# Kernel tuning notes

Measured on AMD Instinct MI355X. Metric: run time of the kernel, lower is better.

Reference implementation:

```python
import jax, jax.numpy as jnp
import numpy as np

B, T, F, H, FW = 4096, 200, 32, 8, 5  # batch, seq, features, hidden, forward_size


def setup_inputs() -> dict:
    key = jax.random.key(0)
    ks = jax.random.split(key, 12)
    s_ih = 1.0 / np.sqrt(F + 1)
    s_hh = 1.0 / np.sqrt(H)
    inp = {
        "x": jax.random.normal(ks[0], (B, T, F), dtype=jnp.float32),
        "z0": jax.random.uniform(ks[1], (1, B, 1), dtype=jnp.float32),
        # LSTM cell over concat([x_t, z_{t-1}]) -> hidden 8, torch gate order i,f,g,o
        "W_ih": jax.random.uniform(ks[2], (4 * H, F + 1), minval=-s_ih, maxval=s_ih),
        "W_hh": jax.random.uniform(ks[3], (4 * H, H), minval=-s_hh, maxval=s_hh),
        "b_ih": jax.random.uniform(ks[4], (4 * H,), minval=-s_hh, maxval=s_hh),
        "b_hh": jax.random.uniform(ks[5], (4 * H,), minval=-s_hh, maxval=s_hh),
        # forward head: 8 -> 5 (relu, dropout inert at inference) -> 1 (relu, monotone increment)
        "W1": jax.random.uniform(ks[6], (FW, H), minval=-s_hh, maxval=s_hh),
        "b1": jax.random.uniform(ks[7], (FW,), minval=-s_hh, maxval=s_hh),
        "W2": jax.random.uniform(ks[8], (1, FW), minval=-1 / np.sqrt(FW), maxval=1 / np.sqrt(FW)),
        "b2": jax.random.uniform(ks[9], (1,), minval=-1 / np.sqrt(FW), maxval=1 / np.sqrt(FW)),
    }
    return inp


def _monotonic_lstm(x, z0, W_ih, W_hh, b_ih, b_hh, W1, b1, W2, b2):
    Bloc = x.shape[0]
    h0 = jnp.zeros((Bloc, H), x.dtype)
    c0 = jnp.zeros((Bloc, H), x.dtype)
    z = z0[0]  # (B, 1) : drop num_layers dim
    bias = b_ih + b_hh

    def step(carry, xt):
        h, c, z = carry
        inp = jnp.concatenate([xt, z], axis=-1)  # (B, F+1)
        gates = inp @ W_ih.T + h @ W_hh.T + bias  # (B, 4H)
        i, f, g, o = jnp.split(gates, 4, axis=-1)
        c = jax.nn.sigmoid(f) * c + jax.nn.sigmoid(i) * jnp.tanh(g)
        h = jax.nn.sigmoid(o) * jnp.tanh(c)
        d = jax.nn.relu(h @ W1.T + b1)            # dropout is identity at inference
        delta = jax.nn.relu(d @ W2.T + b2)        # nonnegative increment -> monotone z
        z = z + delta
        return (h, c, z), z

    _, zs = jax.lax.scan(step, (h0, c0, z), jnp.swapaxes(x, 0, 1))  # zs: (T, B, 1)
    return jnp.swapaxes(zs, 0, 1)  # (B, T, 1)


def reference(x, z0, W_ih, W_hh, b_ih, b_hh, W1, b1, W2, b2):
    return _monotonic_lstm(x, z0, W_ih, W_hh, b_ih, b_hh, W1, b1, W2, b2)
```

## Files before the change

kernel.cpp:

```cpp
#include <hip/hip_runtime.h>

#define T_LEN 200
#define F_IN  32
#define TC    8
#define NCH   (T_LEN / TC)
#define NB    4
#define PSTR  264
#define ZSTR  204

#define QP(a,b,c,d) ((a)|((b)<<2)|((c)<<4)|((d)<<6))
#define DPP_HM 0x141

typedef short  bf16x8  __attribute__((ext_vector_type(8)));
typedef float  floatx4 __attribute__((ext_vector_type(4)));

template <int CTRL>
__device__ __forceinline__ float dppf(float v) {
    return __int_as_float(__builtin_amdgcn_update_dpp(
        0, __float_as_int(v), CTRL, 0xF, 0xF, true));
}
__device__ __forceinline__ void bfsplit(float x, short& hi, short& lo) {
    unsigned u = __float_as_uint(x);
    unsigned short h = (unsigned short)(u >> 16);
    float fh = __uint_as_float(((unsigned)h) << 16);
    float r  = x - fh;
    hi = (short)h;
    lo = (short)(__float_as_uint(r) >> 16);
}

__launch_bounds__(128, 2)
__global__ void mono_lstm_kernel(const float* __restrict__ x,
                                 const float* __restrict__ z0,
                                 const float* __restrict__ W_ih,
                                 const float* __restrict__ W_hh,
                                 const float* __restrict__ b_ih,
                                 const float* __restrict__ b_hh,
                                 const float* __restrict__ W1,
                                 const float* __restrict__ b1,
                                 const float* __restrict__ W2,
                                 const float* __restrict__ b2,
                                 float* __restrict__ out) {
    __shared__ float pls[2 * NB * PSTR];
    __shared__ float zls[NB * ZSTR];

    const int tid  = threadIdx.x;
    const int lane = tid & 63;
    const int wv   = tid >> 6;
    const int bl   = (lane >> 3) & (NB - 1);
    const int j    = lane & 7;
    const int bg   = blockIdx.x * NB;

    const float L2E = 1.4426950408889634f;
    const float NSC = -L2E;
    const float NSG = -2.0f * L2E;

    const int n  = lane & 15;
    const int kq = lane >> 4;
    bf16x8 Bh0, Bl0, Bh1, Bl1;
    float bias0 = 0.f, bias1 = 0.f;

    const int   am  = lane & 15;
    const float* xa = x + ((size_t)(bg + (am >> 2)) * T_LEN + (am & 3)) * F_IN + kq * 8;

    float4 rgv[4];
    auto load_x = [&](int ch) {
#pragma unroll
        for (int s = 0; s < 2; ++s) {
            const float* p = xa + (size_t)(ch * TC + 4 * s) * F_IN;
            rgv[2 * s]     = *(const float4*)p;
            rgv[2 * s + 1] = *(const float4*)(p + 4);
        }
    };
    auto mfma_phase = [&](int buf) {
#pragma unroll
        for (int s = 0; s < 2; ++s) {
            const float xv[8] = {rgv[2*s].x, rgv[2*s].y, rgv[2*s].z, rgv[2*s].w,
                                 rgv[2*s+1].x, rgv[2*s+1].y, rgv[2*s+1].z, rgv[2*s+1].w};
            bf16x8 Ah, Al;
#pragma unroll
            for (int i = 0; i < 8; ++i) {
                short h, l;
                bfsplit(xv[i], h, l);
                Ah[i] = h; Al[i] = l;
            }
            floatx4 a0 = {bias0, bias0, bias0, bias0};
            floatx4 a1 = {bias1, bias1, bias1, bias1};
            a0 = __builtin_amdgcn_mfma_f32_16x16x32_bf16(Ah, Bh0, a0, 0, 0, 0);
            a0 = __builtin_amdgcn_mfma_f32_16x16x32_bf16(Al, Bh0, a0, 0, 0, 0);
            a0 = __builtin_amdgcn_mfma_f32_16x16x32_bf16(Ah, Bl0, a0, 0, 0, 0);
            a1 = __builtin_amdgcn_mfma_f32_16x16x32_bf16(Ah, Bh1, a1, 0, 0, 0);
            a1 = __builtin_amdgcn_mfma_f32_16x16x32_bf16(Al, Bh1, a1, 0, 0, 0);
            a1 = __builtin_amdgcn_mfma_f32_16x16x32_bf16(Ah, Bl1, a1, 0, 0, 0);
#pragma unroll
            for (int reg = 0; reg < 4; ++reg) {
                const int mr = (lane >> 4) * 4 + reg;
                const int bb = mr >> 2, tt = s * 4 + (mr & 3);
                pls[buf * NB * PSTR + bb * PSTR + tt * 32 + n]      = a0[reg];
                pls[buf * NB * PSTR + bb * PSTR + tt * 32 + 16 + n] = a1[reg];
            }
        }
    };

    float whi[8], whf[8], whg[8], who[8];
    float wzi = 0.f, wzf = 0.f, wzg = 0.f, wzo = 0.f;
    float w1h[5][8], b1v[5], w2v[5];
    float b2v = 0.f;
    float ha0 = 0.f, ha1 = 0.f, ha2 = 0.f, ha3 = 0.f,
          ha4 = 0.f, ha5 = 0.f, ha6 = 0.f, ha7 = 0.f;
    float c = 0.0f;
    float z = 0.f;

    if (wv == 1) {
        const int row0 = n, row1 = 16 + n;
        const float sc0 = NSC;
        const float sc1 = (n < 8) ? NSG : NSC;
#pragma unroll
        for (int i = 0; i < 8; ++i) {
            const int k = kq * 8 + i;
            short h, l;
            bfsplit(W_ih[row0 * 33 + k] * sc0, h, l); Bh0[i] = h; Bl0[i] = l;
            bfsplit(W_ih[row1 * 33 + k] * sc1, h, l); Bh1[i] = h; Bl1[i] = l;
        }
        bias0 = (b_ih[row0] + b_hh[row0]) * sc0;
        bias1 = (b_ih[row1] + b_hh[row1]) * sc1;

        load_x(0);
        mfma_phase(0);
        load_x(1);
    } else {
        const int ri = j, rf = 8 + j, rg_ = 16 + j, ro = 24 + j;
#pragma unroll
        for (int k = 0; k < 8; ++k) {
            whi[k] = W_hh[ri * 8 + (j ^ k)] * NSC;
            whf[k] = W_hh[rf * 8 + (j ^ k)] * NSC;
            whg[k] = W_hh[rg_ * 8 + (j ^ k)] * NSG;
            who[k] = W_hh[ro * 8 + (j ^ k)] * NSC;
        }
        wzi = W_ih[ri * 33 + 32] * NSC;
        wzf = W_ih[rf * 33 + 32] * NSC;
        wzg = W_ih[rg_ * 33 + 32] * NSG;
        wzo = W_ih[ro * 33 + 32] * NSC;

#pragma unroll
        for (int m = 0; m < 5; ++m) {
#pragma unroll
            for (int k = 0; k < 8; ++k) w1h[m][k] = W1[m * 8 + (j ^ k)];
            b1v[m] = b1[m];
            w2v[m] = W2[m];
        }
        b2v = b2[0];
        z = z0[bg + bl];
    }

    __syncthreads();

    for (int ch = 0; ch < NCH; ++ch) {
        if (wv == 1) {
            if (ch + 1 < NCH) {
                mfma_phase((ch + 1) & 1);
                if (ch + 2 < NCH) load_x(ch + 2);
            }
        } else {
            const int base = (ch & 1) * NB * PSTR + bl * PSTR;
            float pvi[TC], pvf[TC], pvg[TC], pvo[TC];
#pragma unroll
            for (int t = 0; t < TC; ++t) {
                pvi[t] = pls[base + t * 32 + j];
                pvf[t] = pls[base + t * 32 + 8 + j];
                pvg[t] = pls[base + t * 32 + 16 + j];
                pvo[t] = pls[base + t * 32 + 24 + j];
            }

#pragma unroll
            for (int t = 0; t < TC; ++t) {
                float mi = fmaf(whi[0], ha0, fmaf(whi[1], ha1,
                           fmaf(whi[2], ha2, fmaf(whi[3], ha3, pvi[t]))));
                float ni = fmaf(whi[4], ha4, fmaf(whi[5], ha5,
                           fmaf(whi[6], ha6, whi[7] * ha7)));
                float mf = fmaf(whf[0], ha0, fmaf(whf[1], ha1,
                           fmaf(whf[2], ha2, fmaf(whf[3], ha3, pvf[t]))));
                float nf = fmaf(whf[4], ha4, fmaf(whf[5], ha5,
                           fmaf(whf[6], ha6, whf[7] * ha7)));
                float mg = fmaf(whg[0], ha0, fmaf(whg[1], ha1,
                           fmaf(whg[2], ha2, fmaf(whg[3], ha3, pvg[t]))));
                float ng = fmaf(whg[4], ha4, fmaf(whg[5], ha5,
                           fmaf(whg[6], ha6, whg[7] * ha7)));
                float mo = fmaf(who[0], ha0, fmaf(who[1], ha1,
                           fmaf(who[2], ha2, fmaf(who[3], ha3, pvo[t]))));
                float no = fmaf(who[4], ha4, fmaf(who[5], ha5,
                           fmaf(who[6], ha6, who[7] * ha7)));

                const float ai = fmaf(wzi, z, mi + ni);
                const float af = fmaf(wzf, z, mf + nf);
                const float ag = fmaf(wzg, z, mg + ng);
                const float ao = fmaf(wzo, z, mo + no);

                const float si = __builtin_amdgcn_rcpf(1.0f + __builtin_amdgcn_exp2f(ai));
                const float sf = __builtin_amdgcn_rcpf(1.0f + __builtin_amdgcn_exp2f(af));
                const float sg = __builtin_amdgcn_rcpf(1.0f + __builtin_amdgcn_exp2f(ag));
                const float so = __builtin_amdgcn_rcpf(1.0f + __builtin_amdgcn_exp2f(ao));
                const float tg = fmaf(2.0f, sg, -1.0f);

                c = fmaf(sf, c, si * tg);
                const float ec = __builtin_amdgcn_exp2f(c * (-2.0f * L2E));
                const float tc = fmaf(2.0f, __builtin_amdgcn_rcpf(1.0f + ec), -1.0f);
                const float hn = so * tc;

                ha0 = hn;
                ha1 = dppf<QP(1, 0, 3, 2)>(hn);
                ha2 = dppf<QP(2, 3, 0, 1)>(hn);
                ha3 = dppf<QP(3, 2, 1, 0)>(hn);
                const float t7 = dppf<DPP_HM>(hn);
                ha7 = t7;
                ha4 = dppf<QP(3, 2, 1, 0)>(t7);
                ha5 = dppf<QP(2, 3, 0, 1)>(t7);
                ha6 = dppf<QP(1, 0, 3, 2)>(t7);

                float d0a = fmaf(w1h[0][0], ha0, fmaf(w1h[0][1], ha1, fmaf(w1h[0][2], ha2, b1v[0])));
                float d0b = fmaf(w1h[0][4], ha4, fmaf(w1h[0][5], ha5, fmaf(w1h[0][6], ha6, w1h[0][7] * ha7)));
                float d1a = fmaf(w1h[1][0], ha0, fmaf(w1h[1][1], ha1, fmaf(w1h[1][2], ha2, b1v[1])));
                float d1b = fmaf(w1h[1][4], ha4, fmaf(w1h[1][5], ha5, fmaf(w1h[1][6], ha6, w1h[1][7] * ha7)));
                float d2a = fmaf(w1h[2][0], ha0, fmaf(w1h[2][1], ha1, fmaf(w1h[2][2], ha2, b1v[2])));
                float d2b = fmaf(w1h[2][4], ha4, fmaf(w1h[2][5], ha5, fmaf(w1h[2][6], ha6, w1h[2][7] * ha7)));
                float d3a = fmaf(w1h[3][0], ha0, fmaf(w1h[3][1], ha1, fmaf(w1h[3][2], ha2, b1v[3])));
                float d3b = fmaf(w1h[3][4], ha4, fmaf(w1h[3][5], ha5, fmaf(w1h[3][6], ha6, w1h[3][7] * ha7)));
                float d4a = fmaf(w1h[4][0], ha0, fmaf(w1h[4][1], ha1, fmaf(w1h[4][2], ha2, b1v[4])));
                float d4b = fmaf(w1h[4][4], ha4, fmaf(w1h[4][5], ha5, fmaf(w1h[4][6], ha6, w1h[4][7] * ha7)));
                const float d0 = fmaxf(fmaf(w1h[0][3], ha3, d0a + d0b), 0.0f);
                const float d1 = fmaxf(fmaf(w1h[1][3], ha3, d1a + d1b), 0.0f);
                const float d2 = fmaxf(fmaf(w1h[2][3], ha3, d2a + d2b), 0.0f);
                const float d3 = fmaxf(fmaf(w1h[3][3], ha3, d3a + d3b), 0.0f);
                const float d4 = fmaxf(fmaf(w1h[4][3], ha3, d4a + d4b), 0.0f);
                const float q1 = fmaf(w2v[0], d0, fmaf(w2v[1], d1, b2v));
                const float q2 = fmaf(w2v[2], d2, fmaf(w2v[3], d3, w2v[4] * d4));
                z += fmaxf(q1 + q2, 0.0f);

                if (j == t && lane < 32) zls[bl * ZSTR + ch * TC + t] = z;
            }
        }
        __syncthreads();
    }

#pragma unroll
    for (int it = 0; it < 2; ++it) {
        const int idx = tid + it * 128;
        if (idx < NB * (T_LEN / 4)) {
            const int bb = idx / 50, rem = idx - bb * 50;
            *(float4*)&out[(size_t)(bg + bb) * T_LEN + rem * 4] =
                *(const float4*)&zls[bb * ZSTR + rem * 4];
        }
    }
}

extern "C" void kernel_launch(void* const* d_in, const int* in_sizes, int n_in,
                              void* d_out, int out_size, void* d_ws, size_t ws_size,
                              hipStream_t stream) {
    const float* x    = (const float*)d_in[0];
    const float* z0   = (const float*)d_in[1];
    const float* W_ih = (const float*)d_in[2];
    const float* W_hh = (const float*)d_in[3];
    const float* b_ih = (const float*)d_in[4];
    const float* b_hh = (const float*)d_in[5];
    const float* W1   = (const float*)d_in[6];
    const float* b1   = (const float*)d_in[7];
    const float* W2   = (const float*)d_in[8];
    const float* b2   = (const float*)d_in[9];
    float* out = (float*)d_out;

    const int B = in_sizes[1];
    dim3 grid(B / NB), block(128);
    hipLaunchKernelGGL(mono_lstm_kernel, grid, block, 0, stream,
                       x, z0, W_ih, W_hh, b_ih, b_hh, W1, b1, W2, b2, out);
}
```

Measured before the change: 189.7 us.

## Process sixteen batch rows per block with two interleaved recurrence chains per lane

Raises rows per block from 4 to 16 so each lane of the recurrence wave carries two independent LSTM chains, removing the redundant duplicated lanes and exposing instruction-level parallelism across the serial dependency. The MFMA producer wave now converts twice as many rows per chunk, and z outputs are buffered in registers and written once per chunk instead of per step. The block count drops fourfold and launch bounds allow only one block per CU, so latency hiding relies on in-wave interleaving rather than multiple resident blocks.

```diff
diff --git a/kernel.cpp b/kernel.cpp
--- a/kernel.cpp
+++ b/kernel.cpp
@@ -4,7 +4,7 @@
 #define F_IN  32
 #define TC    8
 #define NCH   (T_LEN / TC)
-#define NB    4
+#define NB    16
 #define PSTR  264
 #define ZSTR  204
 
@@ -28,7 +28,7 @@
     lo = (short)(__float_as_uint(r) >> 16);
 }
 
-__launch_bounds__(128, 2)
+__launch_bounds__(128, 1)
 __global__ void mono_lstm_kernel(const float* __restrict__ x,
                                  const float* __restrict__ z0,
                                  const float* __restrict__ W_ih,
@@ -46,7 +46,7 @@
     const int tid  = threadIdx.x;
     const int lane = tid & 63;
     const int wv   = tid >> 6;
-    const int bl   = (lane >> 3) & (NB - 1);
+    const int bl   = lane >> 3;
     const int j    = lane & 7;
     const int bg   = blockIdx.x * NB;
 
@@ -60,43 +60,51 @@
     float bias0 = 0.f, bias1 = 0.f;
 
     const int   am  = lane & 15;
-    const float* xa = x + ((size_t)(bg + (am >> 2)) * T_LEN + (am & 3)) * F_IN + kq * 8;
-
-    float4 rgv[4];
+    const float* xa0 = x + ((size_t)(bg + (am >> 1)) * T_LEN + (am & 1)) * F_IN + kq * 8;
+    const float* xa1 = xa0 + (size_t)8 * T_LEN * F_IN;
+
+    float4 rgv[2][8];
     auto load_x = [&](int ch) {
 #pragma unroll
-        for (int s = 0; s < 2; ++s) {
-            const float* p = xa + (size_t)(ch * TC + 4 * s) * F_IN;
-            rgv[2 * s]     = *(const float4*)p;
-            rgv[2 * s + 1] = *(const float4*)(p + 4);
+        for (int sub = 0; sub < 2; ++sub) {
+            const float* xa = sub ? xa1 : xa0;
+#pragma unroll
+            for (int s = 0; s < 4; ++s) {
+                const float* p = xa + (size_t)(ch * TC + 2 * s) * F_IN;
+                rgv[sub][2 * s]     = *(const float4*)p;
+                rgv[sub][2 * s + 1] = *(const float4*)(p + 4);
+            }
         }
     };
     auto mfma_phase = [&](int buf) {
 #pragma unroll
-        for (int s = 0; s < 2; ++s) {
-            const float xv[8] = {rgv[2*s].x, rgv[2*s].y, rgv[2*s].z, rgv[2*s].w,
-                                 rgv[2*s+1].x, rgv[2*s+1].y, rgv[2*s+1].z, rgv[2*s+1].w};
-            bf16x8 Ah, Al;
-#pragma unroll
-            for (int i = 0; i < 8; ++i) {
-                short h, l;
-                bfsplit(xv[i], h, l);
-                Ah[i] = h; Al[i] = l;
-            }
-            floatx4 a0 = {bias0, bias0, bias0, bias0};
-            floatx4 a1 = {bias1, bias1, bias1, bias1};
-            a0 = __builtin_amdgcn_mfma_f32_16x16x32_bf16(Ah, Bh0, a0, 0, 0, 0);
-            a0 = __builtin_amdgcn_mfma_f32_16x16x32_bf16(Al, Bh0, a0, 0, 0, 0);
-            a0 = __builtin_amdgcn_mfma_f32_16x16x32_bf16(Ah, Bl0, a0, 0, 0, 0);
-            a1 = __builtin_amdgcn_mfma_f32_16x16x32_bf16(Ah, Bh1, a1, 0, 0, 0);
-            a1 = __builtin_amdgcn_mfma_f32_16x16x32_bf16(Al, Bh1, a1, 0, 0, 0);
-            a1 = __builtin_amdgcn_mfma_f32_16x16x32_bf16(Ah, Bl1, a1, 0, 0, 0);
-#pragma unroll
-            for (int reg = 0; reg < 4; ++reg) {
-                const int mr = (lane >> 4) * 4 + reg;
-                const int bb = mr >> 2, tt = s * 4 + (mr & 3);
-                pls[buf * NB * PSTR + bb * PSTR + tt * 32 + n]      = a0[reg];
-                pls[buf * NB * PSTR + bb * PSTR + tt * 32 + 16 + n] = a1[reg];
+        for (int sub = 0; sub < 2; ++sub) {
+#pragma unroll
+            for (int s = 0; s < 4; ++s) {
+                const float xv[8] = {rgv[sub][2*s].x, rgv[sub][2*s].y, rgv[sub][2*s].z, rgv[sub][2*s].w,
+                                     rgv[sub][2*s+1].x, rgv[sub][2*s+1].y, rgv[sub][2*s+1].z, rgv[sub][2*s+1].w};
+                bf16x8 Ah, Al;
+#pragma unroll
+                for (int i = 0; i < 8; ++i) {
+                    short h, l;
+                    bfsplit(xv[i], h, l);
+                    Ah[i] = h; Al[i] = l;
+                }
+                floatx4 a0 = {bias0, bias0, bias0, bias0};
+                floatx4 a1 = {bias1, bias1, bias1, bias1};
+                a0 = __builtin_amdgcn_mfma_f32_16x16x32_bf16(Ah, Bh0, a0, 0, 0, 0);
+                a0 = __builtin_amdgcn_mfma_f32_16x16x32_bf16(Al, Bh0, a0, 0, 0, 0);
+                a0 = __builtin_amdgcn_mfma_f32_16x16x32_bf16(Ah, Bl0, a0, 0, 0, 0);
+                a1 = __builtin_amdgcn_mfma_f32_16x16x32_bf16(Ah, Bh1, a1, 0, 0, 0);
+                a1 = __builtin_amdgcn_mfma_f32_16x16x32_bf16(Al, Bh1, a1, 0, 0, 0);
+                a1 = __builtin_amdgcn_mfma_f32_16x16x32_bf16(Ah, Bl1, a1, 0, 0, 0);
+#pragma unroll
+                for (int reg = 0; reg < 4; ++reg) {
+                    const int mr = (lane >> 4) * 4 + reg;
+                    const int bb = sub * 8 + (mr >> 1), tt = 2 * s + (mr & 1);
+                    pls[buf * NB * PSTR + bb * PSTR + tt * 32 + n]      = a0[reg];
+                    pls[buf * NB * PSTR + bb * PSTR + tt * 32 + 16 + n] = a1[reg];
+                }
             }
         }
     };
@@ -105,10 +113,14 @@
     float wzi = 0.f, wzf = 0.f, wzg = 0.f, wzo = 0.f;
     float w1h[5][8], b1v[5], w2v[5];
     float b2v = 0.f;
-    float ha0 = 0.f, ha1 = 0.f, ha2 = 0.f, ha3 = 0.f,
-          ha4 = 0.f, ha5 = 0.f, ha6 = 0.f, ha7 = 0.f;
-    float c = 0.0f;
-    float z = 0.f;
+    float ha[2][8];
+    float cst[2] = {0.f, 0.f};
+    float zst[2] = {0.f, 0.f};
+    float zk[2]  = {0.f, 0.f};
+#pragma unroll
+    for (int st = 0; st < 2; ++st)
+#pragma unroll
+        for (int k = 0; k < 8; ++k) ha[st][k] = 0.f;
 
     if (wv == 1) {
         const int row0 = n, row1 = 16 + n;
@@ -149,7 +161,8 @@
             w2v[m] = W2[m];
         }
         b2v = b2[0];
-        z = z0[bg + bl];
+        zst[0] = z0[bg + bl];
+        zst[1] = z0[bg + 8 + bl];
     }
 
     __syncthreads();
@@ -161,88 +174,102 @@
                 if (ch + 2 < NCH) load_x(ch + 2);
             }
         } else {
-            const int base = (ch & 1) * NB * PSTR + bl * PSTR;
-            float pvi[TC], pvf[TC], pvg[TC], pvo[TC];
-#pragma unroll
-            for (int t = 0; t < TC; ++t) {
-                pvi[t] = pls[base + t * 32 + j];
-                pvf[t] = pls[base + t * 32 + 8 + j];
-                pvg[t] = pls[base + t * 32 + 16 + j];
-                pvo[t] = pls[base + t * 32 + 24 + j];
+            const int base = (ch & 1) * NB * PSTR;
+#pragma unroll
+            for (int half = 0; half < 2; ++half) {
+                float pv[2][4][4];
+#pragma unroll
+                for (int st = 0; st < 2; ++st) {
+                    const int rbase = base + (st * 8 + bl) * PSTR;
+#pragma unroll
+                    for (int tt = 0; tt < 4; ++tt) {
+                        const int a = rbase + (half * 4 + tt) * 32 + j;
+                        pv[st][0][tt] = pls[a];
+                        pv[st][1][tt] = pls[a + 8];
+                        pv[st][2][tt] = pls[a + 16];
+                        pv[st][3][tt] = pls[a + 24];
+                    }
+                }
+
+#pragma unroll
+                for (int tt = 0; tt < 4; ++tt) {
+                    const int t = half * 4 + tt;
+#pragma unroll
+                    for (int st = 0; st < 2; ++st) {
+                        float mi = fmaf(whi[0], ha[st][0], fmaf(whi[1], ha[st][1],
+                                   fmaf(whi[2], ha[st][2], fmaf(whi[3], ha[st][3], pv[st][0][tt]))));
+                        float ni = fmaf(whi[4], ha[st][4], fmaf(whi[5], ha[st][5],
+                                   fmaf(whi[6], ha[st][6], whi[7] * ha[st][7])));
+                        float mf = fmaf(whf[0], ha[st][0], fmaf(whf[1], ha[st][1],
+                                   fmaf(whf[2], ha[st][2], fmaf(whf[3], ha[st][3], pv[st][1][tt]))));
+                        float nf = fmaf(whf[4], ha[st][4], fmaf(whf[5], ha[st][5],
+                                   fmaf(whf[6], ha[st][6], whf[7] * ha[st][7])));
+                        float mg = fmaf(whg[0], ha[st][0], fmaf(whg[1], ha[st][1],
+                                   fmaf(whg[2], ha[st][2], fmaf(whg[3], ha[st][3], pv[st][2][tt]))));
+                        float ng = fmaf(whg[4], ha[st][4], fmaf(whg[5], ha[st][5],
+                                   fmaf(whg[6], ha[st][6], whg[7] * ha[st][7])));
+                        float mo = fmaf(who[0], ha[st][0], fmaf(who[1], ha[st][1],
+                                   fmaf(who[2], ha[st][2], fmaf(who[3], ha[st][3], pv[st][3][tt]))));
+                        float no = fmaf(who[4], ha[st][4], fmaf(who[5], ha[st][5],
+                                   fmaf(who[6], ha[st][6], who[7] * ha[st][7])));
+
+                        const float ai = fmaf(wzi, zst[st], mi + ni);
+                        const float af = fmaf(wzf, zst[st], mf + nf);
+                        const float ag = fmaf(wzg, zst[st], mg + ng);
+                        const float ao = fmaf(wzo, zst[st], mo + no);
+
+                        const float si = __builtin_amdgcn_rcpf(1.0f + __builtin_amdgcn_exp2f(ai));
+                        const float sf = __builtin_amdgcn_rcpf(1.0f + __builtin_amdgcn_exp2f(af));
+                        const float sg = __builtin_amdgcn_rcpf(1.0f + __builtin_amdgcn_exp2f(ag));
+                        const float so = __builtin_amdgcn_rcpf(1.0f + __builtin_amdgcn_exp2f(ao));
+                        const float tg = fmaf(2.0f, sg, -1.0f);
+
+                        cst[st] = fmaf(sf, cst[st], si * tg);
+                        const float ec = __builtin_amdgcn_exp2f(cst[st] * (-2.0f * L2E));
+                        const float tc = fmaf(2.0f, __builtin_amdgcn_rcpf(1.0f + ec), -1.0f);
+                        const float hn = so * tc;
+
+                        ha[st][0] = hn;
+                        ha[st][1] = dppf<QP(1, 0, 3, 2)>(hn);
+                        ha[st][2] = dppf<QP(2, 3, 0, 1)>(hn);
+                        ha[st][3] = dppf<QP(3, 2, 1, 0)>(hn);
+                        const float t7 = dppf<DPP_HM>(hn);
+                        ha[st][7] = t7;
+                        ha[st][4] = dppf<QP(3, 2, 1, 0)>(t7);
+                        ha[st][5] = dppf<QP(2, 3, 0, 1)>(t7);
+                        ha[st][6] = dppf<QP(1, 0, 3, 2)>(t7);
+
+                        float d0a = fmaf(w1h[0][0], ha[st][0], fmaf(w1h[0][1], ha[st][1], fmaf(w1h[0][2], ha[st][2], b1v[0])));
+                        float d0b = fmaf(w1h[0][4], ha[st][4], fmaf(w1h[0][5], ha[st][5], fmaf(w1h[0][6], ha[st][6], w1h[0][7] * ha[st][7])));
+                        float d1a = fmaf(w1h[1][0], ha[st][0], fmaf(w1h[1][1], ha[st][1], fmaf(w1h[1][2], ha[st][2], b1v[1])));
+                        float d1b = fmaf(w1h[1][4], ha[st][4], fmaf(w1h[1][5], ha[st][5], fmaf(w1h[1][6], ha[st][6], w1h[1][7] * ha[st][7])));
+                        float d2a = fmaf(w1h[2][0], ha[st][0], fmaf(w1h[2][1], ha[st][1], fmaf(w1h[2][2], ha[st][2], b1v[2])));
+                        float d2b = fmaf(w1h[2][4], ha[st][4], fmaf(w1h[2][5], ha[st][5], fmaf(w1h[2][6], ha[st][6], w1h[2][7] * ha[st][7])));
+                        float d3a = fmaf(w1h[3][0], ha[st][0], fmaf(w1h[3][1], ha[st][1], fmaf(w1h[3][2], ha[st][2], b1v[3])));
+                        float d3b = fmaf(w1h[3][4], ha[st][4], fmaf(w1h[3][5], ha[st][5], fmaf(w1h[3][6], ha[st][6], w1h[3][7] * ha[st][7])));
+                        float d4a = fmaf(w1h[4][0], ha[st][0], fmaf(w1h[4][1], ha[st][1], fmaf(w1h[4][2], ha[st][2], b1v[4])));
+                        float d4b = fmaf(w1h[4][4], ha[st][4], fmaf(w1h[4][5], ha[st][5], fmaf(w1h[4][6], ha[st][6], w1h[4][7] * ha[st][7])));
+                        const float d0 = fmaxf(fmaf(w1h[0][3], ha[st][3], d0a + d0b), 0.0f);
+                        const float d1 = fmaxf(fmaf(w1h[1][3], ha[st][3], d1a + d1b), 0.0f);
+                        const float d2 = fmaxf(fmaf(w1h[2][3], ha[st][3], d2a + d2b), 0.0f);
+                        const float d3 = fmaxf(fmaf(w1h[3][3], ha[st][3], d3a + d3b), 0.0f);
+                        const float d4 = fmaxf(fmaf(w1h[4][3], ha[st][3], d4a + d4b), 0.0f);
+                        const float q1 = fmaf(w2v[0], d0, fmaf(w2v[1], d1, b2v));
+                        const float q2 = fmaf(w2v[2], d2, fmaf(w2v[3], d3, w2v[4] * d4));
+                        zst[st] += fmaxf(q1 + q2, 0.0f);
+
+                        zk[st] = (j == t) ? zst[st] : zk[st];
+                    }
+                }
             }
-
-#pragma unroll
-            for (int t = 0; t < TC; ++t) {
-                float mi = fmaf(whi[0], ha0, fmaf(whi[1], ha1,
-                           fmaf(whi[2], ha2, fmaf(whi[3], ha3, pvi[t]))));
-                float ni = fmaf(whi[4], ha4, fmaf(whi[5], ha5,
-                           fmaf(whi[6], ha6, whi[7] * ha7)));
-                float mf = fmaf(whf[0], ha0, fmaf(whf[1], ha1,
-                           fmaf(whf[2], ha2, fmaf(whf[3], ha3, pvf[t]))));
-                float nf = fmaf(whf[4], ha4, fmaf(whf[5], ha5,
-                           fmaf(whf[6], ha6, whf[7] * ha7)));
-                float mg = fmaf(whg[0], ha0, fmaf(whg[1], ha1,
-                           fmaf(whg[2], ha2, fmaf(whg[3], ha3, pvg[t]))));
-                float ng = fmaf(whg[4], ha4, fmaf(whg[5], ha5,
-                           fmaf(whg[6], ha6, whg[7] * ha7)));
-                float mo = fmaf(who[0], ha0, fmaf(who[1], ha1,
-                           fmaf(who[2], ha2, fmaf(who[3], ha3, pvo[t]))));
-                float no = fmaf(who[4], ha4, fmaf(who[5], ha5,
-                           fmaf(who[6], ha6, who[7] * ha7)));
-
-                const float ai = fmaf(wzi, z, mi + ni);
-                const float af = fmaf(wzf, z, mf + nf);
-                const float ag = fmaf(wzg, z, mg + ng);
-                const float ao = fmaf(wzo, z, mo + no);
-
-                const float si = __builtin_amdgcn_rcpf(1.0f + __builtin_amdgcn_exp2f(ai));
-                const float sf = __builtin_amdgcn_rcpf(1.0f + __builtin_amdgcn_exp2f(af));
-                const float sg = __builtin_amdgcn_rcpf(1.0f + __builtin_amdgcn_exp2f(ag));
-                const float so = __builtin_amdgcn_rcpf(1.0f + __builtin_amdgcn_exp2f(ao));
-                const float tg = fmaf(2.0f, sg, -1.0f);
-
-                c = fmaf(sf, c, si * tg);
-                const float ec = __builtin_amdgcn_exp2f(c * (-2.0f * L2E));
-                const float tc = fmaf(2.0f, __builtin_amdgcn_rcpf(1.0f + ec), -1.0f);
-                const float hn = so * tc;
-
-                ha0 = hn;
-                ha1 = dppf<QP(1, 0, 3, 2)>(hn);
-                ha2 = dppf<QP(2, 3, 0, 1)>(hn);
-                ha3 = dppf<QP(3, 2, 1, 0)>(hn);
-                const float t7 = dppf<DPP_HM>(hn);
-                ha7 = t7;
-                ha4 = dppf<QP(3, 2, 1, 0)>(t7);
-                ha5 = dppf<QP(2, 3, 0, 1)>(t7);
-                ha6 = dppf<QP(1, 0, 3, 2)>(t7);
-
-                float d0a = fmaf(w1h[0][0], ha0, fmaf(w1h[0][1], ha1, fmaf(w1h[0][2], ha2, b1v[0])));
-                float d0b = fmaf(w1h[0][4], ha4, fmaf(w1h[0][5], ha5, fmaf(w1h[0][6], ha6, w1h[0][7] * ha7)));
-                float d1a = fmaf(w1h[1][0], ha0, fmaf(w1h[1][1], ha1, fmaf(w1h[1][2], ha2, b1v[1])));
-                float d1b = fmaf(w1h[1][4], ha4, fmaf(w1h[1][5], ha5, fmaf(w1h[1][6], ha6, w1h[1][7] * ha7)));
-                float d2a = fmaf(w1h[2][0], ha0, fmaf(w1h[2][1], ha1, fmaf(w1h[2][2], ha2, b1v[2])));
-                float d2b = fmaf(w1h[2][4], ha4, fmaf(w1h[2][5], ha5, fmaf(w1h[2][6], ha6, w1h[2][7] * ha7)));
-                float d3a = fmaf(w1h[3][0], ha0, fmaf(w1h[3][1], ha1, fmaf(w1h[3][2], ha2, b1v[3])));
-                float d3b = fmaf(w1h[3][4], ha4, fmaf(w1h[3][5], ha5, fmaf(w1h[3][6], ha6, w1h[3][7] * ha7)));
-                float d4a = fmaf(w1h[4][0], ha0, fmaf(w1h[4][1], ha1, fmaf(w1h[4][2], ha2, b1v[4])));
-                float d4b = fmaf(w1h[4][4], ha4, fmaf(w1h[4][5], ha5, fmaf(w1h[4][6], ha6, w1h[4][7] * ha7)));
-                const float d0 = fmaxf(fmaf(w1h[0][3], ha3, d0a + d0b), 0.0f);
-                const float d1 = fmaxf(fmaf(w1h[1][3], ha3, d1a + d1b), 0.0f);
-                const float d2 = fmaxf(fmaf(w1h[2][3], ha3, d2a + d2b), 0.0f);
-                const float d3 = fmaxf(fmaf(w1h[3][3], ha3, d3a + d3b), 0.0f);
-                const float d4 = fmaxf(fmaf(w1h[4][3], ha3, d4a + d4b), 0.0f);
-                const float q1 = fmaf(w2v[0], d0, fmaf(w2v[1], d1, b2v));
-                const float q2 = fmaf(w2v[2], d2, fmaf(w2v[3], d3, w2v[4] * d4));
-                z += fmaxf(q1 + q2, 0.0f);
-
-                if (j == t && lane < 32) zls[bl * ZSTR + ch * TC + t] = z;
-            }
+            zls[bl * ZSTR + ch * TC + j]        = zk[0];
+            zls[(8 + bl) * ZSTR + ch * TC + j]  = zk[1];
         }
         __syncthreads();
     }
 
 #pragma unroll
-    for (int it = 0; it < 2; ++it) {
+    for (int it = 0; it < 7; ++it) {
         const int idx = tid + it * 128;
         if (idx < NB * (T_LEN / 4)) {
             const int bb = idx / 50, rem = idx - bb * 50;
```

After: 217.5 us. 14.7% more time.
